# Kernel tuning notes

Measured on AMD Instinct MI355X. Metric: run time of the kernel, lower is better.

## Reference

```python
import jax, jax.numpy as jnp
import numpy as np

N, E = 50000, 400000
IN_DIM, HID, OUT = 512, 256, 128


def _lin(key, fan_in, fan_out, bias=True):
    k1, k2 = jax.random.split(key)
    s = 1.0 / np.sqrt(fan_in)
    W = jax.random.uniform(k1, (fan_in, fan_out), minval=-s, maxval=s, dtype=jnp.float32)
    if bias:
        b = jax.random.uniform(k2, (fan_out,), minval=-s, maxval=s, dtype=jnp.float32)
        return W, b
    return W


def setup_inputs() -> dict:
    key = jax.random.key(0)
    ks = jax.random.split(key, 16)
    feature_data = jax.random.normal(ks[0], (N, IN_DIM), dtype=jnp.float32)
    edge_info = jax.random.randint(ks[1], (2, E), 0, N, dtype=jnp.int32)
    W1, b1 = _lin(ks[2], IN_DIM, HID)
    W2, b2 = _lin(ks[3], HID, HID)
    W3, b3 = _lin(ks[4], HID, HID)
    # SAGEConv params: lin_l (aggregated neighbors, with bias), lin_r (root, no bias)
    Wl1, bl1 = _lin(ks[5], HID, HID); Wr1 = _lin(ks[6], HID, HID, bias=False)
    WlH, blH = _lin(ks[7], HID, HID); WrH = _lin(ks[8], HID, HID, bias=False)
    Wl2, bl2 = _lin(ks[9], HID, HID); Wr2 = _lin(ks[10], HID, HID, bias=False)
    Wp1, bp1 = _lin(ks[11], HID, HID)
    Wp2, bp2 = _lin(ks[12], HID, HID)
    Wp3, bp3 = _lin(ks[13], HID, OUT)
    return dict(feature_data=feature_data, edge_info=edge_info,
                W1=W1, b1=b1, W2=W2, b2=b2, W3=W3, b3=b3,
                Wl1=Wl1, bl1=bl1, Wr1=Wr1,
                WlH=WlH, blH=blH, WrH=WrH,
                Wl2=Wl2, bl2=bl2, Wr2=Wr2,
                Wp1=Wp1, bp1=bp1, Wp2=Wp2, bp2=bp2, Wp3=Wp3, bp3=bp3)


def _sage_softmax_conv(x, src, dst, Wl, bl, Wr, n_nodes):
    # messages are source node features
    m = x[src]                                                   # [E, d]
    mx = jax.ops.segment_max(m, dst, num_segments=n_nodes)      # per-dest, per-channel max
    e = jnp.exp(m - mx[dst])                                     # stable softmax numerator
    s = jax.ops.segment_sum(e, dst, num_segments=n_nodes)
    alpha = e / s[dst]                                           # per-dest channel softmax
    aggr = jax.ops.segment_sum(alpha * m, dst, num_segments=n_nodes)  # [N, d]
    return aggr @ Wl + bl + x @ Wr


def reference(feature_data, edge_info,
              W1, b1, W2, b2, W3, b3,
              Wl1, bl1, Wr1, WlH, blH, WrH, Wl2, bl2, Wr2,
              Wp1, bp1, Wp2, bp2, Wp3, bp3):
    n = feature_data.shape[0]
    src, dst = edge_info[0], edge_info[1]
    # eval mode: dropout is identity
    x = jax.nn.relu(feature_data @ W1 + b1)
    x = jax.nn.relu(x @ W2 + b2)
    x = jax.nn.relu(x @ W3 + b3)
    x = jax.nn.relu(_sage_softmax_conv(x, src, dst, Wl1, bl1, Wr1, n))
    x = jax.nn.relu(_sage_softmax_conv(x, src, dst, WlH, blH, WrH, n))
    x = jax.nn.relu(_sage_softmax_conv(x, src, dst, Wl2, bl2, Wr2, n))
    x = jax.nn.relu(x @ Wp1 + bp1)
    x = jax.nn.relu(x @ Wp2 + bp2)
    return jnp.tanh(x @ Wp3 + bp3)
```

## Files before the change

### kernel.cpp

```cpp
#include <hip/hip_runtime.h>
#include <hip/hip_bf16.h>
#include <math.h>

typedef short s8v __attribute__((ext_vector_type(8)));
typedef float f32x4 __attribute__((ext_vector_type(4)));
typedef unsigned u32x4 __attribute__((ext_vector_type(4)));

__device__ __forceinline__ ushort f2bf(float f) {
    __hip_bfloat16 h = __float2bfloat16(f);
    return *reinterpret_cast<ushort*>(&h);
}
__device__ __forceinline__ float bf2f(ushort u) {
    return __uint_as_float(((unsigned)u) << 16);
}
__device__ __forceinline__ unsigned pack_split(float v) {
    ushort h = f2bf(v);
    ushort l = f2bf(v - bf2f(h));
    return ((unsigned)h << 16) | (unsigned)l;
}
__device__ __forceinline__ float unpack_f(unsigned p) {
    return __uint_as_float(p & 0xffff0000u) + __uint_as_float(p << 16);
}
__device__ __forceinline__ void gload16(const void* g, void* l) {
    __builtin_amdgcn_global_load_lds(
        (const __attribute__((address_space(1))) void*)g,
        (__attribute__((address_space(3))) void*)l, 16, 0, 0);
}
__device__ __forceinline__ unsigned lds_addr(const void* p) {
    return (unsigned)(size_t)(const __attribute__((address_space(3))) void*)p;
}
__device__ __forceinline__ void unpack8(const u32x4 p0, const u32x4 p1, s8v& hi, s8v& lo) {
    union { s8v v; unsigned u[4]; } H, L;
    H.u[0] = (p0[0] >> 16) | (p0[1] & 0xffff0000u);
    H.u[1] = (p0[2] >> 16) | (p0[3] & 0xffff0000u);
    H.u[2] = (p1[0] >> 16) | (p1[1] & 0xffff0000u);
    H.u[3] = (p1[2] >> 16) | (p1[3] & 0xffff0000u);
    L.u[0] = (p0[0] & 0xffffu) | (p0[1] << 16);
    L.u[1] = (p0[2] & 0xffffu) | (p0[3] << 16);
    L.u[2] = (p1[0] & 0xffffu) | (p1[1] << 16);
    L.u[3] = (p1[2] & 0xffffu) | (p1[3] << 16);
    hi = H.v; lo = L.v;
}
__device__ __forceinline__ void cvt8(const u32x4 p0, const u32x4 p1, s8v& hi, s8v& lo) {
    union { s8v v; ushort e[8]; } H, L;
    float f[8] = {__uint_as_float(p0[0]), __uint_as_float(p0[1]),
                  __uint_as_float(p0[2]), __uint_as_float(p0[3]),
                  __uint_as_float(p1[0]), __uint_as_float(p1[1]),
                  __uint_as_float(p1[2]), __uint_as_float(p1[3])};
    #pragma unroll
    for (int e = 0; e < 8; ++e) {
        ushort h = f2bf(f[e]);
        H.e[e] = (ushort)h;
        L.e[e] = f2bf(f[e] - bf2f(h));
    }
    hi = H.v; lo = L.v;
}
template<bool AF32>
__device__ __forceinline__ void frag_a(const u32x4 p0, const u32x4 p1, s8v& hi, s8v& lo) {
    if constexpr (AF32) cvt8(p0, p1, hi, lo);
    else                unpack8(p0, p1, hi, lo);
}

#define DSR(dst, addr, OFF) \
    asm volatile("ds_read_b128 %0, %1 offset:" #OFF : "=v"(dst) : "v"(addr))

#define TRI(ah, al, bh, bl, C) \
    C = __builtin_amdgcn_mfma_f32_16x16x32_bf16(ah, bh, C, 0, 0, 0); \
    C = __builtin_amdgcn_mfma_f32_16x16x32_bf16(ah, bl, C, 0, 0, 0); \
    C = __builtin_amdgcn_mfma_f32_16x16x32_bf16(al, bh, C, 0, 0, 0);


__global__ __launch_bounds__(256)
void hist_kernel(const int* __restrict__ dst, int* __restrict__ cnt, int E) {
    int e = blockIdx.x * 256 + threadIdx.x;
    if (e < E) atomicAdd(&cnt[dst[e]], 1);
}

__global__ __launch_bounds__(256)
void scan_part(const int* __restrict__ cnt, int* __restrict__ bsum, int n) {
    __shared__ int s[256];
    int b = blockIdx.x, t = threadIdx.x;
    int i0 = b * 1024 + t * 4;
    int v = 0;
    if (i0 + 3 < n) {
        int4 q = *(const int4*)(cnt + i0);
        v = q.x + q.y + q.z + q.w;
    } else {
        for (int i = 0; i < 4; ++i) if (i0 + i < n) v += cnt[i0 + i];
    }
    s[t] = v;
    __syncthreads();
    for (int d = 128; d > 0; d >>= 1) {
        if (t < d) s[t] += s[t + d];
        __syncthreads();
    }
    if (t == 0) bsum[b] = s[0];
}

__global__ __launch_bounds__(64)
void scan_top(int* __restrict__ bsum, int nb) {
    int l = threadIdx.x;
    int own = (l < nb) ? bsum[l] : 0;
    int v = own;
    #pragma unroll
    for (int d = 1; d < 64; d <<= 1) {
        int u = __shfl_up(v, d, 64);
        if (l >= d) v += u;
    }
    if (l < nb) bsum[l] = v - own;
}

__global__ __launch_bounds__(256)
void scan_final(const int* __restrict__ cnt, const int* __restrict__ bsum,
                int* __restrict__ off, int n, int E) {
    __shared__ int s[256];
    int b = blockIdx.x, t = threadIdx.x;
    int i0 = b * 1024 + t * 4;
    int v0 = 0, v1 = 0, v2 = 0, v3 = 0;
    if (i0 + 3 < n) {
        int4 q = *(const int4*)(cnt + i0);
        v0 = q.x; v1 = q.y; v2 = q.z; v3 = q.w;
    } else {
        if (i0     < n) v0 = cnt[i0];
        if (i0 + 1 < n) v1 = cnt[i0 + 1];
        if (i0 + 2 < n) v2 = cnt[i0 + 2];
        if (i0 + 3 < n) v3 = cnt[i0 + 3];
    }
    int tsum = v0 + v1 + v2 + v3;
    s[t] = tsum;
    __syncthreads();
    for (int d = 1; d < 256; d <<= 1) {
        int u = (t >= d) ? s[t - d] : 0;
        __syncthreads();
        s[t] += u;
        __syncthreads();
    }
    int excl = s[t] - tsum + bsum[b];
    if (i0     < n) off[i0]     = excl;
    if (i0 + 1 < n) off[i0 + 1] = excl + v0;
    if (i0 + 2 < n) off[i0 + 2] = excl + v0 + v1;
    if (i0 + 3 < n) off[i0 + 3] = excl + v0 + v1 + v2;
    if (b == 0 && t == 0) off[n] = E;
}

__global__ __launch_bounds__(256)
void scatter_kernel(const int* __restrict__ src, const int* __restrict__ dst,
                    int* __restrict__ cur, const int* __restrict__ off,
                    int* __restrict__ csr, int E) {
    int e = blockIdx.x * 256 + threadIdx.x;
    if (e < E) {
        int d = dst[e];
        int pos = off[d] + atomicAdd(&cur[d], 1);
        csr[pos] = src[e];
    }
}


struct PrepW {
    const float* W[12];
    unsigned* D[12];
    int end[12];
    int stride[12];
    int koff[12];
    int nshift[12];
};

__global__ __launch_bounds__(256)
void prep_weights(PrepW a, int total) {
    int id = blockIdx.x * 256 + threadIdx.x;
    if (id >= total) return;
    int s = 0;
    #pragma unroll
    for (int i = 0; i < 12; ++i) if (id >= a.end[i]) s = i + 1;
    int base = (s == 0) ? 0 : a.end[s - 1];
    int e = id - base;
    int Nmask = (1 << a.nshift[s]) - 1;
    int n = e & Nmask;
    int k = e >> a.nshift[s];
    float w = a.W[s][(size_t)k * (Nmask + 1) + n];
    a.D[s][(size_t)n * a.stride[s] + a.koff[s] + k] = pack_split(w);
}


__global__ __launch_bounds__(256)
void sage_aggr_pk(const unsigned* __restrict__ X, const int* __restrict__ csr,
                  const int* __restrict__ off, unsigned* __restrict__ O, int nN) {
    int node = blockIdx.x * 4 + (threadIdx.x >> 6);
    if (node >= nN) return;
    int c4 = (threadIdx.x & 63) * 4;
    int s0 = off[node], s1 = off[node + 1];
    float se0 = 0, se1 = 0, se2 = 0, se3 = 0;
    float sm0 = 0, sm1 = 0, sm2 = 0, sm3 = 0;
    for (int j = s0; j < s1; ++j) {
        uint4 p = *(const uint4*)(X + (size_t)csr[j] * 256 + c4);
        float v0 = unpack_f(p.x), v1 = unpack_f(p.y), v2 = unpack_f(p.z), v3 = unpack_f(p.w);
        float e0 = __expf(fminf(v0, 60.f));
        float e1 = __expf(fminf(v1, 60.f));
        float e2 = __expf(fminf(v2, 60.f));
        float e3 = __expf(fminf(v3, 60.f));
        se0 += e0; sm0 = fmaf(v0, e0, sm0);
        se1 += e1; sm1 = fmaf(v1, e1, sm1);
        se2 += e2; sm2 = fmaf(v2, e2, sm2);
        se3 += e3; sm3 = fmaf(v3, e3, sm3);
    }
    uint4 o;
    o.x = pack_split((s1 > s0) ? sm0 / se0 : 0.f);
    o.y = pack_split((s1 > s0) ? sm1 / se1 : 0.f);
    o.z = pack_split((s1 > s0) ? sm2 / se2 : 0.f);
    o.w = pack_split((s1 > s0) ? sm3 / se3 : 0.f);
    *(uint4*)(O + (size_t)node * 256 + c4) = o;
}


template<int NT1, int NT2, bool AF32, int NB, bool DOTANH>
__global__ __launch_bounds__(512, 2)
void gemm_pipe(const float* __restrict__ A1f, const unsigned* __restrict__ A1,
               const unsigned* __restrict__ A2,
               const unsigned* __restrict__ B,
               const float* __restrict__ bias,
               unsigned* __restrict__ Cpk, float* __restrict__ Cf, int M) {
    constexpr int NT = NT1 + NT2;
    constexpr int KU = NT * 32;
    __shared__ unsigned lds[3][12288];

    const int tid = threadIdx.x;
    const int l = tid & 63;
    const int w = tid >> 6;
    const int wm = w >> 2, wn = w & 3;
    const int li = l & 15, kq = l >> 4;
    const int bm = blockIdx.x * 128;

    const int srow = 8 * w + (l >> 3);
    const int schunk = (l & 7) ^ (l >> 3);

    const unsigned lbase = lds_addr(&lds[0][0]);
    const unsigned swz0 = (unsigned)((((2 * kq)) ^ (li & 7)) * 16);
    const unsigned aoff = (unsigned)((wm * 64 + li) * 128) + swz0;
    const unsigned boff = 16384u + (unsigned)((wn * 64 + li) * 128) + swz0;

    f32x4 acc[4][4];
    #pragma unroll
    for (int i = 0; i < 4; ++i)
        #pragma unroll
        for (int j = 0; j < 4; ++j) acc[i][j] = (f32x4){0.f, 0.f, 0.f, 0.f};

    auto STAGE = [&](int t, int buf) {
        #pragma unroll
        for (int s = 0; s < 2; ++s) {
            int r = 64 * s + srow;
            int gr = bm + r; gr = (gr < M) ? gr : (M - 1);
            const void* src;
            if constexpr (AF32) {
                src = A1f + (size_t)gr * KU + t * 32 + schunk * 4;
            } else if constexpr (NT2 > 0) {
                src = (t < NT1) ? (const void*)(A1 + (size_t)gr * (NT1 * 32) + t * 32 + schunk * 4)
                                : (const void*)(A2 + (size_t)gr * (NT2 * 32) + (t - NT1) * 32 + schunk * 4);
            } else {
                src = A1 + (size_t)gr * KU + t * 32 + schunk * 4;
            }
            gload16(src, &lds[buf][s * 2048 + w * 256 + l * 4]);
        }
        #pragma unroll
        for (int s = 0; s < 4; ++s) {
            int n = 64 * s + srow;
            int gn = (n < NB) ? n : (NB - 1);
            const unsigned* src = B + (size_t)gn * KU + t * 32 + schunk * 4;
            gload16(src, &lds[buf][4096 + s * 2048 + w * 256 + l * 4]);
        }
    };

    STAGE(0, 0);
    STAGE(1, 1);

    #pragma unroll
    for (int t = 0; t < NT; ++t) {
        if (t + 1 < NT) asm volatile("s_waitcnt vmcnt(6)" ::: "memory");
        else            asm volatile("s_waitcnt vmcnt(0)" ::: "memory");
        __builtin_amdgcn_s_barrier();

        const int buf = t % 3;
        const unsigned lb = lbase + (unsigned)buf * 49152u;
        unsigned ab = lb + aoff, bb = lb + boff;
        unsigned ab1 = ab ^ 16u, bb1 = bb ^ 16u;

        u32x4 B0, B1, B2, B3, B4, B5, B6, B7;
        u32x4 A0, A4, A1v, A5, A2v, A6, A3, A7;
        DSR(B0, bb, 0);    DSR(B1, bb, 2048);  DSR(B2, bb, 4096);  DSR(B3, bb, 6144);
        DSR(B4, bb1, 0);   DSR(B5, bb1, 2048); DSR(B6, bb1, 4096); DSR(B7, bb1, 6144);
        DSR(A0, ab, 0);    DSR(A4, ab1, 0);
        __builtin_amdgcn_sched_barrier(0);

        if (t + 2 < NT) STAGE(t + 2, (t + 2) % 3);
        __builtin_amdgcn_sched_barrier(0);

        DSR(A1v, ab, 2048); DSR(A5, ab1, 2048);
        asm volatile("s_waitcnt lgkmcnt(2)" ::: "memory");
        __builtin_amdgcn_sched_barrier(0);

        s8v bh0, bl0, bh1, bl1, bh2, bl2, bh3, bl3;
        unpack8(B0, B4, bh0, bl0);
        unpack8(B1, B5, bh1, bl1);
        unpack8(B2, B6, bh2, bl2);
        unpack8(B3, B7, bh3, bl3);

        __builtin_amdgcn_s_setprio(1);
        {
            s8v ah, al;
            frag_a<AF32>(A0, A4, ah, al);
            TRI(ah, al, bh0, bl0, acc[0][0]) TRI(ah, al, bh1, bl1, acc[0][1])
            TRI(ah, al, bh2, bl2, acc[0][2]) TRI(ah, al, bh3, bl3, acc[0][3])
        }
        __builtin_amdgcn_sched_barrier(0);
        DSR(A2v, ab, 4096); DSR(A6, ab1, 4096);
        asm volatile("s_waitcnt lgkmcnt(2)" ::: "memory");
        __builtin_amdgcn_sched_barrier(0);
        {
            s8v ah, al;
            frag_a<AF32>(A1v, A5, ah, al);
            TRI(ah, al, bh0, bl0, acc[1][0]) TRI(ah, al, bh1, bl1, acc[1][1])
            TRI(ah, al, bh2, bl2, acc[1][2]) TRI(ah, al, bh3, bl3, acc[1][3])
        }
        __builtin_amdgcn_sched_barrier(0);
        DSR(A3, ab, 6144); DSR(A7, ab1, 6144);
        asm volatile("s_waitcnt lgkmcnt(2)" ::: "memory");
        __builtin_amdgcn_sched_barrier(0);
        {
            s8v ah, al;
            frag_a<AF32>(A2v, A6, ah, al);
            TRI(ah, al, bh0, bl0, acc[2][0]) TRI(ah, al, bh1, bl1, acc[2][1])
            TRI(ah, al, bh2, bl2, acc[2][2]) TRI(ah, al, bh3, bl3, acc[2][3])
        }
        asm volatile("s_waitcnt lgkmcnt(0)" ::: "memory");
        __builtin_amdgcn_sched_barrier(0);
        {
            s8v ah, al;
            frag_a<AF32>(A3, A7, ah, al);
            TRI(ah, al, bh0, bl0, acc[3][0]) TRI(ah, al, bh1, bl1, acc[3][1])
            TRI(ah, al, bh2, bl2, acc[3][2]) TRI(ah, al, bh3, bl3, acc[3][3])
        }
        __builtin_amdgcn_s_setprio(0);
    }

    #pragma unroll
    for (int j = 0; j < 4; ++j) {
        int col = wn * 64 + 16 * j + li;
        float b = bias[(col < NB) ? col : 0];
        #pragma unroll
        for (int i = 0; i < 4; ++i) {
            int row0 = bm + wm * 64 + 16 * i + kq * 4;
            #pragma unroll
            for (int r = 0; r < 4; ++r) {
                float v = acc[i][j][r] + b;
                if constexpr (DOTANH) {
                    if (row0 + r < M && col < NB)
                        Cf[(size_t)(row0 + r) * NB + col] = tanhf(v);
                } else {
                    Cpk[(size_t)(row0 + r) * 256 + col] = pack_split(fmaxf(v, 0.f));
                }
            }
        }
    }
}


extern "C" void kernel_launch(void* const* d_in, const int* in_sizes, int n_in,
                              void* d_out, int out_size, void* d_ws, size_t ws_size,
                              hipStream_t stream) {
    const float* feat = (const float*)d_in[0];
    const int* einfo = (const int*)d_in[1];
    const float* b1 = (const float*)d_in[3];
    const float* b2 = (const float*)d_in[5];
    const float* b3 = (const float*)d_in[7];
    const float* bl1 = (const float*)d_in[9];
    const float* blH = (const float*)d_in[12];
    const float* bl2 = (const float*)d_in[15];
    const float* bp1 = (const float*)d_in[18];
    const float* bp2 = (const float*)d_in[20];
    const float* bp3 = (const float*)d_in[22];

    const int IN_DIM = 512;
    const int N = in_sizes[0] / IN_DIM;
    const int E = in_sizes[1] / 2;
    const int* src = einfo;
    const int* dst = einfo + E;
    const int M_pad = ((N + 127) / 128) * 128;
    const size_t PLANE_U = (size_t)M_pad * 256;

    unsigned* P0 = (unsigned*)d_ws;
    unsigned* P1 = P0 + PLANE_U;
    unsigned* P2 = P1 + PLANE_U;
    unsigned* wp = P2 + PLANE_U;

    const int gsz[9] = {131072, 65536, 65536, 131072, 131072, 131072, 65536, 65536, 32768};
    unsigned* G[9];
    {
        unsigned* c = wp;
        for (int i = 0; i < 9; ++i) { G[i] = c; c += gsz[i]; }
        wp = c;
    }

    const int widx[12]   = {2, 4, 6, 8, 10, 11, 13, 14, 16, 17, 19, 21};
    const int wplane[12] = {0, 1, 2, 3, 3, 4, 4, 5, 5, 6, 7, 8};
    const int wstr[12]   = {512, 256, 256, 512, 512, 512, 512, 512, 512, 256, 256, 256};
    const int wkoff[12]  = {0, 0, 0, 0, 256, 0, 256, 0, 256, 0, 0, 0};
    const int wnsh[12]   = {8, 8, 8, 8, 8, 8, 8, 8, 8, 8, 8, 7};
    const int welem[12]  = {131072, 65536, 65536, 65536, 65536, 65536, 65536,
                            65536, 65536, 65536, 65536, 32768};

    PrepW pa;
    int acc_end = 0;
    for (int i = 0; i < 12; ++i) {
        pa.W[i] = (const float*)d_in[widx[i]];
        pa.D[i] = G[wplane[i]];
        pa.stride[i] = wstr[i];
        pa.koff[i] = wkoff[i];
        pa.nshift[i] = wnsh[i];
        acc_end += welem[i];
        pa.end[i] = acc_end;
    }

    int* ioff = (int*)wp;
    int* icnt = ioff + ((N + 1 + 3) & ~3);
    int* icur = icnt + ((N + 3) & ~3);
    int* csr  = icur + ((N + 3) & ~3);
    int* bsum = csr + ((E + 3) & ~3);

    const int NBLK = (N + 1023) / 1024;

    hipMemsetAsync(icnt, 0, (size_t)N * sizeof(int), stream);
    hipMemsetAsync(icur, 0, (size_t)N * sizeof(int), stream);
    hist_kernel<<<(E + 255) / 256, 256, 0, stream>>>(dst, icnt, E);
    scan_part<<<NBLK, 256, 0, stream>>>(icnt, bsum, N);
    scan_top<<<1, 64, 0, stream>>>(bsum, NBLK);
    scan_final<<<NBLK, 256, 0, stream>>>(icnt, bsum, ioff, N, E);
    scatter_kernel<<<(E + 255) / 256, 256, 0, stream>>>(src, dst, icur, ioff, csr, E);
    prep_weights<<<(acc_end + 255) / 256, 256, 0, stream>>>(pa, acc_end);

    const int GB = M_pad / 128;
    const int GA = (N + 3) / 4;

    gemm_pipe<16, 0, true, 256, false><<<GB, 512, 0, stream>>>(
        feat, nullptr, nullptr, G[0], b1, P0, nullptr, N);
    gemm_pipe<8, 0, false, 256, false><<<GB, 512, 0, stream>>>(
        nullptr, P0, nullptr, G[1], b2, P1, nullptr, N);
    gemm_pipe<8, 0, false, 256, false><<<GB, 512, 0, stream>>>(
        nullptr, P1, nullptr, G[2], b3, P0, nullptr, N);

    sage_aggr_pk<<<GA, 256, 0, stream>>>(P0, csr, ioff, P1, N);
    gemm_pipe<8, 8, false, 256, false><<<GB, 512, 0, stream>>>(
        nullptr, P1, P0, G[3], bl1, P2, nullptr, N);

    sage_aggr_pk<<<GA, 256, 0, stream>>>(P2, csr, ioff, P1, N);
    gemm_pipe<8, 8, false, 256, false><<<GB, 512, 0, stream>>>(
        nullptr, P1, P2, G[4], blH, P0, nullptr, N);

    sage_aggr_pk<<<GA, 256, 0, stream>>>(P0, csr, ioff, P1, N);
    gemm_pipe<8, 8, false, 256, false><<<GB, 512, 0, stream>>>(
        nullptr, P1, P0, G[5], bl2, P2, nullptr, N);

    gemm_pipe<8, 0, false, 256, false><<<GB, 512, 0, stream>>>(
        nullptr, P2, nullptr, G[6], bp1, P0, nullptr, N);
    gemm_pipe<8, 0, false, 256, false><<<GB, 512, 0, stream>>>(
        nullptr, P0, nullptr, G[7], bp2, P1, nullptr, N);
    gemm_pipe<8, 0, false, 128, true><<<GB, 512, 0, stream>>>(
        nullptr, P1, nullptr, G[8], bp3, nullptr, (float*)d_out, N);
}
```

Baseline: 654.8 us.

## Split GEMM into 128x128 tiles and load weight fragments directly from global

The GEMM now uses 256-thread blocks, each computing a 128x128 output tile, so the grid covers both M and N tiles. B (weight) fragments are prepacked by prep_weights into separate hi/lo bf16 planes in an MFMA-friendly k-major layout. Each wave loads them straight into registers with inline global_load_dwordx4, prefetching one k-step ahead, instead of staging them through LDS and unpacking. This cuts LDS traffic and footprint so more blocks can fit per CU, but it re-reads weights from L2 per tile and relies on hand-written vmcnt accounting.

```diff
diff --git a/kernel.cpp b/kernel.cpp
--- a/kernel.cpp
+++ b/kernel.cpp
@@ -63,6 +63,10 @@
 
 #define DSR(dst, addr, OFF) \
     asm volatile("ds_read_b128 %0, %1 offset:" #OFF : "=v"(dst) : "v"(addr))
+
+#define GLB(dst, voff, base, OFF) \
+    asm volatile("global_load_dwordx4 %0, %1, %2 offset:" #OFF \
+                 : "=v"(dst) : "v"(voff), "s"(base))
 
 #define TRI(ah, al, bh, bl, C) \
     C = __builtin_amdgcn_mfma_f32_16x16x32_bf16(ah, bh, C, 0, 0, 0); \
@@ -158,9 +162,9 @@
 
 struct PrepW {
     const float* W[12];
-    unsigned* D[12];
+    ushort* H[12];
+    ushort* L[12];
     int end[12];
-    int stride[12];
     int koff[12];
     int nshift[12];
 };
@@ -178,7 +182,11 @@
     int n = e & Nmask;
     int k = e >> a.nshift[s];
     float w = a.W[s][(size_t)k * (Nmask + 1) + n];
-    a.D[s][(size_t)n * a.stride[s] + a.koff[s] + k] = pack_split(w);
+    ushort hi = f2bf(w);
+    int kp = a.koff[s] + k;
+    size_t idx = ((size_t)(kp >> 3) * (Nmask + 1) + n) * 8 + (kp & 7);
+    a.H[s][idx] = hi;
+    a.L[s][idx] = f2bf(w - bf2f(hi));
 }
 
 
@@ -213,30 +221,32 @@
 
 
 template<int NT1, int NT2, bool AF32, int NB, bool DOTANH>
-__global__ __launch_bounds__(512, 2)
-void gemm_pipe(const float* __restrict__ A1f, const unsigned* __restrict__ A1,
-               const unsigned* __restrict__ A2,
-               const unsigned* __restrict__ B,
+__global__ __launch_bounds__(256, 3)
+void gemm_pipe(const float* __restrict__ Af,
+               const unsigned* __restrict__ A1, const unsigned* __restrict__ A2,
+               const ushort* __restrict__ BH, const ushort* __restrict__ BL,
                const float* __restrict__ bias,
                unsigned* __restrict__ Cpk, float* __restrict__ Cf, int M) {
     constexpr int NT = NT1 + NT2;
     constexpr int KU = NT * 32;
-    __shared__ unsigned lds[3][12288];
+    constexpr int NCB = NB / 128;
+    constexpr unsigned DSTEP = 4u * NB * 16u;
+    __shared__ unsigned lds[3][4096];
 
     const int tid = threadIdx.x;
     const int l = tid & 63;
     const int w = tid >> 6;
-    const int wm = w >> 2, wn = w & 3;
+    const int wm = w >> 1, wn = w & 1;
     const int li = l & 15, kq = l >> 4;
-    const int bm = blockIdx.x * 128;
-
-    const int srow = 8 * w + (l >> 3);
-    const int schunk = (l & 7) ^ (l >> 3);
+    const int b = blockIdx.x;
+    const int bm = (b / NCB) * 128;
+    const int bn = (b % NCB) * 128;
+
+    const int srow8 = l >> 3;
+    const int schunk = (l & 7) ^ srow8;
 
     const unsigned lbase = lds_addr(&lds[0][0]);
-    const unsigned swz0 = (unsigned)((((2 * kq)) ^ (li & 7)) * 16);
-    const unsigned aoff = (unsigned)((wm * 64 + li) * 128) + swz0;
-    const unsigned boff = 16384u + (unsigned)((wn * 64 + li) * 128) + swz0;
+    const unsigned aoff = (unsigned)((wm * 64 + li) * 128 + (((2 * kq) ^ (li & 7)) * 16));
 
     f32x4 acc[4][4];
     #pragma unroll
@@ -246,62 +256,54 @@
 
     auto STAGE = [&](int t, int buf) {
         #pragma unroll
-        for (int s = 0; s < 2; ++s) {
-            int r = 64 * s + srow;
+        for (int s = 0; s < 4; ++s) {
+            int r = 32 * w + 8 * s + srow8;
             int gr = bm + r; gr = (gr < M) ? gr : (M - 1);
             const void* src;
             if constexpr (AF32) {
-                src = A1f + (size_t)gr * KU + t * 32 + schunk * 4;
+                src = Af + (size_t)gr * KU + t * 32 + schunk * 4;
             } else if constexpr (NT2 > 0) {
                 src = (t < NT1) ? (const void*)(A1 + (size_t)gr * (NT1 * 32) + t * 32 + schunk * 4)
                                 : (const void*)(A2 + (size_t)gr * (NT2 * 32) + (t - NT1) * 32 + schunk * 4);
             } else {
                 src = A1 + (size_t)gr * KU + t * 32 + schunk * 4;
             }
-            gload16(src, &lds[buf][s * 2048 + w * 256 + l * 4]);
-        }
-        #pragma unroll
-        for (int s = 0; s < 4; ++s) {
-            int n = 64 * s + srow;
-            int gn = (n < NB) ? n : (NB - 1);
-            const unsigned* src = B + (size_t)gn * KU + t * 32 + schunk * 4;
-            gload16(src, &lds[buf][4096 + s * 2048 + w * 256 + l * 4]);
+            gload16(src, &lds[buf][(32 * w + 8 * s) * 32 + l * 4]);
         }
     };
+
+    unsigned bv = (unsigned)((kq * NB + bn + wn * 64 + li) * 16);
+    s8v bh0, bh1, bh2, bh3, bl0, bl1, bl2, bl3;
 
     STAGE(0, 0);
     STAGE(1, 1);
+    GLB(bh0, bv, BH, 0);   GLB(bh1, bv, BH, 256);
+    GLB(bh2, bv, BH, 512); GLB(bh3, bv, BH, 768);
+    GLB(bl0, bv, BL, 0);   GLB(bl1, bv, BL, 256);
+    GLB(bl2, bv, BL, 512); GLB(bl3, bv, BL, 768);
+    bv += DSTEP;
+    asm volatile("s_waitcnt vmcnt(8)" ::: "memory");
+    __builtin_amdgcn_sched_barrier(0);
 
     #pragma unroll
     for (int t = 0; t < NT; ++t) {
-        if (t + 1 < NT) asm volatile("s_waitcnt vmcnt(6)" ::: "memory");
-        else            asm volatile("s_waitcnt vmcnt(0)" ::: "memory");
         __builtin_amdgcn_s_barrier();
 
         const int buf = t % 3;
-        const unsigned lb = lbase + (unsigned)buf * 49152u;
-        unsigned ab = lb + aoff, bb = lb + boff;
-        unsigned ab1 = ab ^ 16u, bb1 = bb ^ 16u;
-
-        u32x4 B0, B1, B2, B3, B4, B5, B6, B7;
+        unsigned ab = lbase + (unsigned)buf * 16384u + aoff;
+        unsigned ab1 = ab ^ 16u;
+
         u32x4 A0, A4, A1v, A5, A2v, A6, A3, A7;
-        DSR(B0, bb, 0);    DSR(B1, bb, 2048);  DSR(B2, bb, 4096);  DSR(B3, bb, 6144);
-        DSR(B4, bb1, 0);   DSR(B5, bb1, 2048); DSR(B6, bb1, 4096); DSR(B7, bb1, 6144);
-        DSR(A0, ab, 0);    DSR(A4, ab1, 0);
+        DSR(A0, ab, 0); DSR(A4, ab1, 0);
         __builtin_amdgcn_sched_barrier(0);
 
         if (t + 2 < NT) STAGE(t + 2, (t + 2) % 3);
         __builtin_amdgcn_sched_barrier(0);
 
         DSR(A1v, ab, 2048); DSR(A5, ab1, 2048);
-        asm volatile("s_waitcnt lgkmcnt(2)" ::: "memory");
-        __builtin_amdgcn_sched_barrier(0);
-
-        s8v bh0, bl0, bh1, bl1, bh2, bl2, bh3, bl3;
-        unpack8(B0, B4, bh0, bl0);
-        unpack8(B1, B5, bh1, bl1);
-        unpack8(B2, B6, bh2, bl2);
-        unpack8(B3, B7, bh3, bl3);
+        if (t + 2 < NT) asm volatile("s_waitcnt vmcnt(4) lgkmcnt(2)" ::: "memory");
+        else            asm volatile("s_waitcnt vmcnt(0) lgkmcnt(2)" ::: "memory");
+        __builtin_amdgcn_sched_barrier(0);
 
         __builtin_amdgcn_s_setprio(1);
         {
@@ -339,20 +341,29 @@
             TRI(ah, al, bh2, bl2, acc[3][2]) TRI(ah, al, bh3, bl3, acc[3][3])
         }
         __builtin_amdgcn_s_setprio(0);
+        __builtin_amdgcn_sched_barrier(0);
+
+        if (t + 1 < NT) {
+            GLB(bh0, bv, BH, 0);   GLB(bh1, bv, BH, 256);
+            GLB(bh2, bv, BH, 512); GLB(bh3, bv, BH, 768);
+            GLB(bl0, bv, BL, 0);   GLB(bl1, bv, BL, 256);
+            GLB(bl2, bv, BL, 512); GLB(bl3, bv, BL, 768);
+            bv += DSTEP;
+        }
     }
 
     #pragma unroll
     for (int j = 0; j < 4; ++j) {
-        int col = wn * 64 + 16 * j + li;
-        float b = bias[(col < NB) ? col : 0];
+        int col = bn + wn * 64 + 16 * j + li;
+        float bb = bias[col];
         #pragma unroll
         for (int i = 0; i < 4; ++i) {
             int row0 = bm + wm * 64 + 16 * i + kq * 4;
             #pragma unroll
             for (int r = 0; r < 4; ++r) {
-                float v = acc[i][j][r] + b;
+                float v = acc[i][j][r] + bb;
                 if constexpr (DOTANH) {
-                    if (row0 + r < M && col < NB)
+                    if (row0 + r < M)
                         Cf[(size_t)(row0 + r) * NB + col] = tanhf(v);
                 } else {
                     Cpk[(size_t)(row0 + r) * 256 + col] = pack_split(fmaxf(v, 0.f));
@@ -389,19 +400,14 @@
     unsigned* P0 = (unsigned*)d_ws;
     unsigned* P1 = P0 + PLANE_U;
     unsigned* P2 = P1 + PLANE_U;
-    unsigned* wp = P2 + PLANE_U;
+    ushort* W = (ushort*)(P2 + PLANE_U);
 
     const int gsz[9] = {131072, 65536, 65536, 131072, 131072, 131072, 65536, 65536, 32768};
-    unsigned* G[9];
-    {
-        unsigned* c = wp;
-        for (int i = 0; i < 9; ++i) { G[i] = c; c += gsz[i]; }
-        wp = c;
-    }
+    ushort* GH[9]; ushort* GL[9];
+    for (int i = 0; i < 9; ++i) { GH[i] = W; W += gsz[i]; GL[i] = W; W += gsz[i]; }
 
     const int widx[12]   = {2, 4, 6, 8, 10, 11, 13, 14, 16, 17, 19, 21};
     const int wplane[12] = {0, 1, 2, 3, 3, 4, 4, 5, 5, 6, 7, 8};
-    const int wstr[12]   = {512, 256, 256, 512, 512, 512, 512, 512, 512, 256, 256, 256};
     const int wkoff[12]  = {0, 0, 0, 0, 256, 0, 256, 0, 256, 0, 0, 0};
     const int wnsh[12]   = {8, 8, 8, 8, 8, 8, 8, 8, 8, 8, 8, 7};
     const int welem[12]  = {131072, 65536, 65536, 65536, 65536, 65536, 65536,
@@ -411,15 +417,15 @@
     int acc_end = 0;
     for (int i = 0; i < 12; ++i) {
         pa.W[i] = (const float*)d_in[widx[i]];
-        pa.D[i] = G[wplane[i]];
-        pa.stride[i] = wstr[i];
+        pa.H[i] = GH[wplane[i]];
+        pa.L[i] = GL[wplane[i]];
         pa.koff[i] = wkoff[i];
         pa.nshift[i] = wnsh[i];
         acc_end += welem[i];
         pa.end[i] = acc_end;
     }
 
-    int* ioff = (int*)wp;
+    int* ioff = (int*)(((size_t)W + 15) & ~(size_t)15);
     int* icnt = ioff + ((N + 1 + 3) & ~3);
     int* icur = icnt + ((N + 3) & ~3);
     int* csr  = icur + ((N + 3) & ~3);
@@ -436,32 +442,33 @@
     scatter_kernel<<<(E + 255) / 256, 256, 0, stream>>>(src, dst, icur, ioff, csr, E);
     prep_weights<<<(acc_end + 255) / 256, 256, 0, stream>>>(pa, acc_end);
 
-    const int GB = M_pad / 128;
+    const int GB2 = (M_pad / 128) * 2;
+    const int GB1 = M_pad / 128;
     const int GA = (N + 3) / 4;
 
-    gemm_pipe<16, 0, true, 256, false><<<GB, 512, 0, stream>>>(
-        feat, nullptr, nullptr, G[0], b1, P0, nullptr, N);
-    gemm_pipe<8, 0, false, 256, false><<<GB, 512, 0, stream>>>(
-        nullptr, P0, nullptr, G[1], b2, P1, nullptr, N);
-    gemm_pipe<8, 0, false, 256, false><<<GB, 512, 0, stream>>>(
-        nullptr, P1, nullptr, G[2], b3, P0, nullptr, N);
+    gemm_pipe<16, 0, true, 256, false><<<GB2, 256, 0, stream>>>(
+        feat, nullptr, nullptr, GH[0], GL[0], b1, P0, nullptr, N);
+    gemm_pipe<8, 0, false, 256, false><<<GB2, 256, 0, stream>>>(
+        nullptr, P0, nullptr, GH[1], GL[1], b2, P1, nullptr, N);
+    gemm_pipe<8, 0, false, 256, false><<<GB2, 256, 0, stream>>>(
+        nullptr, P1, nullptr, GH[2], GL[2], b3, P0, nullptr, N);
 
     sage_aggr_pk<<<GA, 256, 0, stream>>>(P0, csr, ioff, P1, N);
-    gemm_pipe<8, 8, false, 256, false><<<GB, 512, 0, stream>>>(
-        nullptr, P1, P0, G[3], bl1, P2, nullptr, N);
+    gemm_pipe<8, 8, false, 256, false><<<GB2, 256, 0, stream>>>(
+        nullptr, P1, P0, GH[3], GL[3], bl1, P2, nullptr, N);
 
     sage_aggr_pk<<<GA, 256, 0, stream>>>(P2, csr, ioff, P1, N);
-    gemm_pipe<8, 8, false, 256, false><<<GB, 512, 0, stream>>>(
-        nullptr, P1, P2, G[4], blH, P0, nullptr, N);
+    gemm_pipe<8, 8, false, 256, false><<<GB2, 256, 0, stream>>>(
+        nullptr, P1, P2, GH[4], GL[4], blH, P0, nullptr, N);
 
     sage_aggr_pk<<<GA, 256, 0, stream>>>(P0, csr, ioff, P1, N);
-    gemm_pipe<8, 8, false, 256, false><<<GB, 512, 0, stream>>>(
-        nullptr, P1, P0, G[5], bl2, P2, nullptr, N);
-
-    gemm_pipe<8, 0, false, 256, false><<<GB, 512, 0, stream>>>(
-        nullptr, P2, nullptr, G[6], bp1, P0, nullptr, N);
-    gemm_pipe<8, 0, false, 256, false><<<GB, 512, 0, stream>>>(
-        nullptr, P0, nullptr, G[7], bp2, P1, nullptr, N);
-    gemm_pipe<8, 0, false, 128, true><<<GB, 512, 0, stream>>>(
-        nullptr, P1, nullptr, G[8], bp3, nullptr, (float*)d_out, N);
-}
+    gemm_pipe<8, 8, false, 256, false><<<GB2, 256, 0, stream>>>(
+        nullptr, P1, P0, GH[5], GL[5], bl2, P2, nullptr, N);
+
+    gemm_pipe<8, 0, false, 256, false><<<GB2, 256, 0, stream>>>(
+        nullptr, P2, nullptr, GH[6], GL[6], bp1, P0, nullptr, N);
+    gemm_pipe<8, 0, false, 256, false><<<GB2, 256, 0, stream>>>(
+        nullptr, P0, nullptr, GH[7], GL[7], bp2, P1, nullptr, N);
+    gemm_pipe<8, 0, false, 128, true><<<GB1, 256, 0, stream>>>(
+        nullptr, P1, nullptr, GH[8], GL[8], bp3, nullptr, (float*)d_out, N);
+}
```

Measured after the change: 626.1 us. 4.4% less time.
